# Performance work log

Hardware: AMD Instinct MI355X
Metric: run time of the kernel (lower is better)

The kernel has to match this reference:

```python
import jax, jax.numpy as jnp
import numpy as np
from jax import lax

H = 256       # GRU/LSTM hidden size
E = 32        # word embedding dim
VOCAB = 128000
MAX_EP = 1000
P_LEN, C_LEN, N_LEN = 512, 256, 512
FH = FW = 6
IMG_FLAT = 64 * FH * FW  # 2304


def _gru(xs, wih, whh, bih, bhh):
    # torch nn.GRU semantics, gate order [r; z; n]; xs: (T, E) -> (T, H)
    gi = xs @ wih.T + bih  # (T, 3H), precompute input projections
    def step(h, g):
        gh = h @ whh.T + bhh
        ir, iz, inn = jnp.split(g, 3)
        hr, hz, hn = jnp.split(gh, 3)
        r = jax.nn.sigmoid(ir + hr)
        z = jax.nn.sigmoid(iz + hz)
        n = jnp.tanh(inn + r * hn)
        h2 = (1.0 - z) * n + z * h
        return h2, h2
    _, hs = lax.scan(step, jnp.zeros((H,), xs.dtype), gi)
    return hs


def _conv(x, w, b, s):
    y = lax.conv_general_dilated(x, w, (s, s), 'VALID',
                                 dimension_numbers=('NCHW', 'OIHW', 'NCHW'))
    return y + b[None, :, None, None]


def setup_inputs() -> dict:
    key = jax.random.key(0)
    ks = iter(jax.random.split(key, 64))
    def w(shape, s=0.02):
        return jax.random.normal(next(ks), shape, jnp.float32) * s
    inp = {}
    inp['x'] = jax.random.normal(next(ks), (1, 3, 124, 124), jnp.float32)
    inp['hx'] = jax.random.normal(next(ks), (1, H), jnp.float32) * 0.1
    inp['cx'] = jax.random.normal(next(ks), (1, H), jnp.float32) * 0.1
    inp['prev_inst'] = jax.random.randint(next(ks), (1, P_LEN), 0, VOCAB)
    inp['curr_inst'] = jax.random.randint(next(ks), (1, C_LEN), 0, VOCAB)
    inp['next_inst'] = jax.random.randint(next(ks), (1, N_LEN), 0, VOCAB)
    inp['tx'] = jax.random.randint(next(ks), (1,), 0, MAX_EP + 1)
    # parameters
    inp['emb'] = w((VOCAB, E), 0.05)
    # GRU order: [f_prev, f_curr, f_next, b_prev, b_curr, b_next]
    inp['gru_wih'] = w((6, 3 * H, E))
    inp['gru_whh'] = w((6, 3 * H, H))
    inp['gru_bih'] = w((6, 3 * H), 0.01)
    inp['gru_bhh'] = w((6, 3 * H), 0.01)
    inp['conv1_w'] = w((128, 3, 8, 8));   inp['conv1_b'] = w((128,), 0.01)
    inp['conv2_w'] = w((64, 128, 4, 4));  inp['conv2_b'] = w((64,), 0.01)
    inp['conv3_w'] = w((64, 64, 4, 4));   inp['conv3_b'] = w((64,), 0.01)
    inp['img_w'] = w((256, IMG_FLAT));    inp['img_b'] = w((256,), 0.01)
    inp['akp_w'] = w((256, 768));         inp['akp_b'] = w((256,), 0.01)
    inp['akn_w'] = w((256, 768));         inp['akn_b'] = w((256,), 0.01)
    inp['bil_p_w'] = w((1, 256, 512));    inp['bil_p_b'] = w((1,), 0.01)
    inp['bil_n_w'] = w((1, 256, 512));    inp['bil_n_b'] = w((1,), 0.01)
    inp['pred_w'] = w((64, 512));         inp['pred_b'] = w((64,), 0.01)
    inp['nred_w'] = w((64, 512));         inp['nred_b'] = w((64,), 0.01)
    inp['gate_w'] = w((64, 512 + 128));   inp['gate_b'] = w((64,), 0.01)
    inp['lin_w'] = w((256, IMG_FLAT));    inp['lin_b'] = w((256,), 0.01)
    inp['lstm_wih'] = w((4 * H, 256));    inp['lstm_whh'] = w((4 * H, H))
    inp['lstm_bih'] = jnp.zeros((4 * H,), jnp.float32)
    inp['lstm_bhh'] = jnp.zeros((4 * H,), jnp.float32)
    inp['time_emb'] = w((MAX_EP + 1, E), 0.05)
    inp['crit_w'] = w((1, 256 + E));      inp['crit_b'] = jnp.zeros((1,), jnp.float32)
    inp['act_w'] = w((4, 256 + E), 0.01); inp['act_b'] = jnp.zeros((4,), jnp.float32)
    return inp


def reference(x, hx, cx, prev_inst, curr_inst, next_inst, tx, emb,
              gru_wih, gru_whh, gru_bih, gru_bhh,
              conv1_w, conv1_b, conv2_w, conv2_b, conv3_w, conv3_b,
              img_w, img_b, akp_w, akp_b, akn_w, akn_b,
              bil_p_w, bil_p_b, bil_n_w, bil_n_b,
              pred_w, pred_b, nred_w, nred_b, gate_w, gate_b,
              lin_w, lin_b, lstm_wih, lstm_whh, lstm_bih, lstm_bhh,
              time_emb, crit_w, crit_b, act_w, act_b):
    # CNN tower
    x1 = jax.nn.relu(_conv(x, conv1_w, conv1_b, 4))
    x2 = jax.nn.relu(_conv(x1, conv2_w, conv2_b, 2))
    x_img = jax.nn.relu(_conv(x2, conv3_w, conv3_b, 2))  # (1,64,6,6)

    ep = emb[prev_inst[0]]  # (P, E)
    ec = emb[curr_inst[0]]  # (C, E)
    en = emb[next_inst[0]]  # (N, E)
    P, C, N = ep.shape[0], ec.shape[0], en.shape[0]

    def run(j, e):
        return _gru(e, gru_wih[j], gru_whh[j], gru_bih[j], gru_bhh[j])
    hf = jnp.concatenate([run(0, ep), run(1, ec), run(2, en)], 0)  # (T, H)
    hb = jnp.concatenate([run(3, ep), run(4, ec), run(5, en)], 0)
    rb = hb[::-1]  # source reverses only the collected hidden list

    curr_rep = jnp.concatenate([hf[P + C - 1], rb[P]])[None]        # (1, 512)
    prev_rep = jnp.concatenate([hf[:P], rb[:P]], 1)                  # (P, 512)
    next_rep = jnp.concatenate([hf[P + C:], rb[P + C:]], 1)          # (N, 512)

    image_emb = x_img.reshape(1, -1) @ img_w.T + img_b               # (1, 256)
    ak_in = jnp.concatenate([curr_rep, image_emb], 1)                # (1, 768)

    def attend(ak_w, ak_b, bw, bb, rep):
        k = (ak_in @ ak_w.T + ak_b)[0]           # (256,) shared key
        s = (k @ bw[0]) @ rep.T + bb[0]          # (L,) bilinear scores
        wgt = jax.nn.softmax(s)
        return wgt @ rep                          # (512,)

    prev_sum = attend(akp_w, akp_b, bil_p_w, bil_p_b, prev_rep)
    next_sum = attend(akn_w, akn_b, bil_n_w, bil_n_b, next_rep)
    pg = prev_sum @ pred_w.T + pred_b            # (64,)
    ng = next_sum @ nred_w.T + nred_b            # (64,)

    gate_in = jnp.concatenate([curr_rep[0], pg, ng])[None]  # (1, 640)
    gate = jax.nn.sigmoid(gate_in @ gate_w.T + gate_b)      # (1, 64)

    xg = (x_img * gate[:, :, None, None]).reshape(1, -1)
    feat = jax.nn.relu(xg @ lin_w.T + lin_b)                # (1, 256)

    # torch LSTMCell, gate order [i; f; g; o]
    g = feat @ lstm_wih.T + lstm_bih + hx @ lstm_whh.T + lstm_bhh
    i, f, gg, o = jnp.split(g, 4, axis=1)
    cx2 = jax.nn.sigmoid(f) * cx + jax.nn.sigmoid(i) * jnp.tanh(gg)
    hx2 = jax.nn.sigmoid(o) * jnp.tanh(cx2)

    te = time_emb[tx].reshape(1, E)
    z = jnp.concatenate([hx2, te], 1)                       # (1, 288)
    return (z @ crit_w.T + crit_b, z @ act_w.T + act_b, hx2, cx2)
```

## Files before the change

### kernel.cpp

```cpp
#include <hip/hip_runtime.h>
#include <hip/hip_bf16.h>

typedef unsigned int u32;
typedef _Float16 f16x8 __attribute__((ext_vector_type(8)));
typedef float f32x4 __attribute__((ext_vector_type(4)));

__device__ __forceinline__ float sigf(float x){ return 1.0f/(1.0f + __expf(-x)); }
__device__ __forceinline__ float tanhfast(float x){
  float xc = fminf(fmaxf(x, -15.0f), 15.0f);
  float e = __expf(2.0f*xc);
  return (e - 1.0f)/(e + 1.0f);
}

#define GI_OFF   0
#define GI_SZ    (2560*768)
#define HF_OFF   (GI_OFF + GI_SZ)
#define HF_SZ    (1280*256)
#define HB_OFF   (HF_OFF + HF_SZ)
#define X1_OFF   (HB_OFF + HF_SZ)
#define X1_SZ    (128*30*30)
#define X2_OFF   (X1_OFF + X1_SZ)
#define X2_SZ    (64*14*14)
#define XIMG_OFF (X2_OFF + X2_SZ)
#define XIMG_SZ  (64*6*6)
#define AKIN_OFF (XIMG_OFF + XIMG_SZ)
#define PSUM_OFF (AKIN_OFF + 768)
#define NSUM_OFF (PSUM_OFF + 512)
#define GATE_OFF (NSUM_OFF + 512)
#define FEAT_OFF (GATE_OFF + 64)
#define G_OFF    (FEAT_OFF + 256)

__global__ __launch_bounds__(256) void gi_kernel(
    const float* __restrict__ emb, const float* __restrict__ wih_all,
    const float* __restrict__ bih_all,
    const int* __restrict__ prev, const int* __restrict__ curr, const int* __restrict__ nxt,
    float* __restrict__ gi_all)
{
  const int offs[7] = {0,512,768,1280,1792,2048,2560};
  int row0 = blockIdx.x * 16;
  int j = 0;
  while (row0 >= offs[j+1]) ++j;
  int t0 = row0 - offs[j];
  int sel = j % 3;
  const int* inst = (sel==0)? prev : (sel==1)? curr : nxt;

  __shared__ __align__(16) float e[16][32];
  int u = threadIdx.x;
  for (int idx=u; idx<512; idx+=256){
    int r = idx >> 5, k = idx & 31;
    e[r][k] = emb[(size_t)inst[t0+r]*32 + k];
  }
  __syncthreads();

  const float* wih = wih_all + (size_t)j*768*32;
  const float* bih = bih_all + (size_t)j*768;
  for (int g3=0; g3<3; ++g3){
    int o = g3*256 + u;
    float bb = bih[o];
    float acc[16];
#pragma unroll
    for (int r=0;r<16;++r) acc[r]=bb;
    const float* wr = wih + (size_t)o*32;
#pragma unroll
    for (int k=0;k<32;++k){
      float w = wr[k];
#pragma unroll
      for (int r=0;r<16;++r) acc[r] += w * e[r][k];
    }
    for (int r=0;r<16;++r) gi_all[(size_t)(row0+r)*768 + o] = acc[r];
  }
}

__global__ __launch_bounds__(256,1) void gru_scan_kernel(
    const float* __restrict__ whh_all, const float* __restrict__ bhh_all,
    const float* __restrict__ gi_all, float* __restrict__ hf, float* __restrict__ hb)
{
  const int lens[6] = {512,256,512,512,256,512};
  const int offs[6] = {0,512,768,1280,1792,2048};
  int j = blockIdx.x;
  int u = threadIdx.x;
  int len = lens[j];
  const float* gi = gi_all + (size_t)offs[j]*768;
  float* outp = ((j<3)? hf : hb) + (size_t)offs[j%3]*256;

  int w    = u >> 6;
  int l    = u & 63;
  int arow = l & 15;
  int kgrp = l >> 4;

  f16x8 af[12][8];
  {
    const float* Wj = whh_all + (size_t)j*768*256;
#pragma unroll
    for (int i=0;i<12;++i){
      const float* wrow = Wj + (size_t)(16*(w*12+i) + arow)*256;
#pragma unroll
      for (int kt=0;kt<8;++kt){
        const float4* p = (const float4*)(wrow + 32*kt + 8*kgrp);
        float4 c0 = p[0], c1 = p[1];
        f16x8 v;
        v[0]=(_Float16)c0.x; v[1]=(_Float16)c0.y; v[2]=(_Float16)c0.z; v[3]=(_Float16)c0.w;
        v[4]=(_Float16)c1.x; v[5]=(_Float16)c1.y; v[6]=(_Float16)c1.z; v[7]=(_Float16)c1.w;
        af[i][kt] = v;
      }
    }
  }

  float bh0 = bhh_all[j*768 + u];
  float bh1 = bhh_all[j*768 + 256 + u];
  float bh2 = bhh_all[j*768 + 512 + u];
  float hprev = 0.0f;

  __shared__ __align__(16) _Float16 h16[256];
  __shared__ __align__(16) float gacc[768];
  h16[u] = (_Float16)0.0f;
  __syncthreads();

  for (int t=0; t<len; ++t){
    if (t > 0) outp[(size_t)(t-1)*256 + u] = hprev;
    const float* git = gi + (size_t)t*768;
    float gr = git[u], gz = git[256+u], gn = git[512+u];

#pragma unroll
    for (int g=0; g<3; ++g){
      f32x4 acc[4];
#pragma unroll
      for (int i=0;i<4;++i){ f32x4 zz = {0.f,0.f,0.f,0.f}; acc[i] = zz; }
#pragma unroll
      for (int kt=0; kt<8; ++kt){
        f16x8 bfr = *(const f16x8*)(h16 + 32*kt + 8*kgrp);
#pragma unroll
        for (int i=0;i<4;++i)
          acc[i] = __builtin_amdgcn_mfma_f32_16x16x32_f16(af[g*4+i][kt], bfr, acc[i], 0, 0, 0);
      }
      if (arow == 0){
#pragma unroll
        for (int i=0;i<4;++i){
          float4 v; v.x=acc[i][0]; v.y=acc[i][1]; v.z=acc[i][2]; v.w=acc[i][3];
          *(float4*)&gacc[16*(w*12 + g*4 + i) + 4*kgrp] = v;
        }
      }
    }
    __syncthreads();

    float r  = sigf(gr + bh0 + gacc[u]);
    float z  = sigf(gz + bh1 + gacc[256+u]);
    float n  = tanhfast(gn + bh2 + r*gacc[512+u]);
    float h2 = (1.0f - z)*n + z*hprev;
    h16[u] = (_Float16)h2;
    hprev = h2;
    __syncthreads();
  }
  outp[(size_t)(len-1)*256 + u] = hprev;
}

__global__ __launch_bounds__(256) void conv1_kernel(
    const float* __restrict__ x, const float* __restrict__ w, const float* __restrict__ b,
    float* __restrict__ y)
{
  int idx = blockIdx.x*256 + threadIdx.x;
  if (idx >= 128*30*30) return;
  int c = idx/900, rem = idx%900, i = rem/30, jx = rem%30;
  float acc = b[c];
  const float* wc = w + (size_t)c*3*8*8;
  for (int ic=0; ic<3; ++ic)
    for (int ky=0; ky<8; ++ky){
      const float* xrow = x + ((size_t)ic*124 + (i*4+ky))*124 + jx*4;
      const float* wrow = wc + (ic*8+ky)*8;
#pragma unroll
      for (int kx=0; kx<8; ++kx) acc += xrow[kx] * wrow[kx];
    }
  y[idx] = fmaxf(acc, 0.0f);
}

__global__ __launch_bounds__(256) void conv2_kernel(
    const float* __restrict__ x1, const float* __restrict__ w, const float* __restrict__ b,
    float* __restrict__ y)
{
  int idx = blockIdx.x*256 + threadIdx.x;
  if (idx >= 64*14*14) return;
  int c = idx/196, rem = idx%196, i = rem/14, jx = rem%14;
  float acc = b[c];
  for (int ic=0; ic<128; ++ic){
    const float* xc = x1 + (size_t)ic*900;
    const float* wc = w + ((size_t)c*128 + ic)*16;
#pragma unroll
    for (int ky=0; ky<4; ++ky)
#pragma unroll
      for (int kx=0; kx<4; ++kx)
        acc += xc[(i*2+ky)*30 + (jx*2+kx)] * wc[ky*4+kx];
  }
  y[idx] = fmaxf(acc, 0.0f);
}

__global__ __launch_bounds__(256) void conv3_kernel(
    const float* __restrict__ x2, const float* __restrict__ w, const float* __restrict__ b,
    float* __restrict__ y)
{
  int idx = blockIdx.x*256 + threadIdx.x;
  if (idx >= 64*6*6) return;
  int c = idx/36, rem = idx%36, i = rem/6, jx = rem%6;
  float acc = b[c];
  for (int ic=0; ic<64; ++ic){
    const float* xc = x2 + (size_t)ic*196;
    const float* wc = w + ((size_t)c*64 + ic)*16;
#pragma unroll
    for (int ky=0; ky<4; ++ky)
#pragma unroll
      for (int kx=0; kx<4; ++kx)
        acc += xc[(i*2+ky)*14 + (jx*2+kx)] * wc[ky*4+kx];
  }
  y[idx] = fmaxf(acc, 0.0f);
}

__global__ __launch_bounds__(256) void imgemb_kernel(
    const float* __restrict__ x_img, const float* __restrict__ img_w, const float* __restrict__ img_b,
    const float* __restrict__ hf, const float* __restrict__ hb, float* __restrict__ ak_in)
{
  int u = threadIdx.x;
  int r = blockIdx.x*8 + (u>>5);
  int lane = u & 31;
  const float* wr = img_w + (size_t)r*2304;
  float acc = 0.0f;
  for (int k=lane; k<2304; k+=32) acc += wr[k]*x_img[k];
#pragma unroll
  for (int m=16; m; m>>=1) acc += __shfl_xor(acc, m, 64);
  if (lane == 0) ak_in[512+r] = img_b[r] + acc;
  if (blockIdx.x == 0){
    ak_in[u]     = hf[(size_t)767*256+u];
    ak_in[256+u] = hb[(size_t)767*256+u];
  }
}

__global__ __launch_bounds__(512) void attend_kernel(
    const float* __restrict__ ak_in_g,
    const float* __restrict__ akp_w, const float* __restrict__ akp_b,
    const float* __restrict__ akn_w, const float* __restrict__ akn_b,
    const float* __restrict__ bil_p_w, const float* __restrict__ bil_p_b,
    const float* __restrict__ bil_n_w, const float* __restrict__ bil_n_b,
    const float* __restrict__ hf, const float* __restrict__ hb,
    float* __restrict__ prev_sum, float* __restrict__ next_sum)
{
  int blk = blockIdx.x;
  const float* akw = blk? akn_w : akp_w;
  const float* akb = blk? akn_b : akp_b;
  const float* bw  = blk? bil_n_w : bil_p_w;
  float bb         = blk? bil_n_b[0] : bil_p_b[0];
  float* outp      = blk? next_sum : prev_sum;

  int u = threadIdx.x;
  __shared__ __align__(16) float ak[768];
  __shared__ __align__(16) float kk[256];
  __shared__ __align__(16) float q[512];
  __shared__ float s[512], red[512];

  for (int i=u; i<768; i+=512) ak[i] = ak_in_g[i];
  __syncthreads();

  if (u < 256){
    float a0=0.f,a1=0.f,a2=0.f,a3=0.f;
    const float4* wr = (const float4*)(akw + (size_t)u*768);
    const float4* av = (const float4*)ak;
    for (int m=0; m<192; ++m){
      float4 w = wr[m], aa = av[m];
      a0 += w.x*aa.x; a1 += w.y*aa.y; a2 += w.z*aa.z; a3 += w.w*aa.w;
    }
    kk[u] = akb[u] + ((a0+a1)+(a2+a3));
  }
  __syncthreads();

  {
    float acc = 0.0f;
    for (int m=0; m<256; ++m) acc += kk[m]*bw[(size_t)m*512 + u];
    q[u] = acc;
  }
  __syncthreads();

  {
    int i = u;
    const float4* repf = (const float4*)(hf + (size_t)(blk? (768+i) : i)*256);
    const float4* repb = (const float4*)(hb + (size_t)(blk? (511-i) : (1279-i))*256);
    const float4* qf = (const float4*)q;
    float a0=0.f,a1=0.f;
    for (int v=0; v<64; ++v){
      float4 qq = qf[v],  rr = repf[v];
      a0 += qq.x*rr.x + qq.y*rr.y + qq.z*rr.z + qq.w*rr.w;
      float4 q2 = qf[64+v], r2 = repb[v];
      a1 += q2.x*r2.x + q2.y*r2.y + q2.z*r2.z + q2.w*r2.w;
    }
    s[u] = bb + a0 + a1;
  }
  __syncthreads();

  red[u] = s[u]; __syncthreads();
  for (int st=256; st>0; st>>=1){ if (u<st) red[u]=fmaxf(red[u],red[u+st]); __syncthreads(); }
  float mx = red[0]; __syncthreads();
  float ex = __expf(s[u]-mx);
  red[u] = ex; __syncthreads();
  for (int st=256; st>0; st>>=1){ if (u<st) red[u]+=red[u+st]; __syncthreads(); }
  float inv = 1.0f/red[0]; __syncthreads();
  s[u] = ex*inv;
  __syncthreads();

  float o = 0.0f;
  if (u < 256){
    for (int r=0; r<512; ++r){
      const float* rf = hf + (size_t)(blk? (768+r) : r)*256;
      o += s[r]*rf[u];
    }
    outp[u] = o;
  } else {
    int v = u-256;
    for (int r=0; r<512; ++r){
      const float* rb = hb + (size_t)(blk? (511-r) : (1279-r))*256;
      o += s[r]*rb[v];
    }
    outp[u] = o;
  }
}

__global__ __launch_bounds__(256) void head_a_kernel(
    const float* __restrict__ psum, const float* __restrict__ nsum,
    const float* __restrict__ akin,
    const float* __restrict__ pred_w, const float* __restrict__ pred_b,
    const float* __restrict__ nred_w, const float* __restrict__ nred_b,
    const float* __restrict__ gate_w, const float* __restrict__ gate_b,
    float* __restrict__ gate_out)
{
  int u = threadIdx.x;
  __shared__ __align__(16) float ps[512], ns[512], cr[512];
  __shared__ float pg[64], ng[64];
  for (int i=u; i<512; i+=256){ ps[i]=psum[i]; ns[i]=nsum[i]; cr[i]=akin[i]; }
  __syncthreads();

  if (u < 64){
    float a = pred_b[u];
    const float* wr = pred_w + (size_t)u*512;
    for (int k=0;k<512;++k) a += ps[k]*wr[k];
    pg[u] = a;
  } else if (u < 128){
    int t = u-64;
    float a = nred_b[t];
    const float* wr = nred_w + (size_t)t*512;
    for (int k=0;k<512;++k) a += ns[k]*wr[k];
    ng[t] = a;
  }
  __syncthreads();

  if (u < 64){
    float a = gate_b[u];
    const float* wr = gate_w + (size_t)u*640;
    for (int k=0;k<512;++k) a += cr[k]*wr[k];
    for (int k=0;k<64;++k)  a += pg[k]*wr[512+k];
    for (int k=0;k<64;++k)  a += ng[k]*wr[576+k];
    gate_out[u] = sigf(a);
  }
}

__global__ __launch_bounds__(256) void lin_kernel(
    const float* __restrict__ x_img, const float* __restrict__ gate,
    const float* __restrict__ lin_w, const float* __restrict__ lin_b,
    float* __restrict__ feat)
{
  int u = threadIdx.x;
  __shared__ __align__(16) float xg[2304];
  for (int i=u; i<2304; i+=256) xg[i] = x_img[i]*gate[i/36];
  __syncthreads();

  int r = blockIdx.x*8 + (u>>5);
  int lane = u & 31;
  const float* wr = lin_w + (size_t)r*2304;
  float acc = 0.0f;
  for (int k=lane; k<2304; k+=32) acc += wr[k]*xg[k];
#pragma unroll
  for (int m=16; m; m>>=1) acc += __shfl_xor(acc, m, 64);
  if (lane == 0) feat[r] = fmaxf(lin_b[r] + acc, 0.0f);
}

__global__ __launch_bounds__(256) void lstm_kernel(
    const float* __restrict__ feat, const float* __restrict__ hx,
    const float* __restrict__ wih, const float* __restrict__ whh,
    const float* __restrict__ bih, const float* __restrict__ bhh,
    float* __restrict__ g)
{
  int u = threadIdx.x;
  __shared__ __align__(16) float fs[256], hs[256];
  fs[u] = feat[u]; hs[u] = hx[u];
  __syncthreads();
  int row = blockIdx.x*256 + u;
  float a0=0.f, a1=0.f;
  const float4* w1 = (const float4*)(wih + (size_t)row*256);
  const float4* w2 = (const float4*)(whh + (size_t)row*256);
  const float4* fv = (const float4*)fs;
  const float4* hv = (const float4*)hs;
  for (int k=0;k<64;++k){
    float4 wa = w1[k], fa = fv[k];
    a0 += wa.x*fa.x + wa.y*fa.y + wa.z*fa.z + wa.w*fa.w;
    float4 wb = w2[k], ha = hv[k];
    a1 += wb.x*ha.x + wb.y*ha.y + wb.z*ha.z + wb.w*ha.w;
  }
  g[row] = bih[row] + bhh[row] + a0 + a1;
}

__global__ __launch_bounds__(320) void final_kernel(
    const float* __restrict__ g, const float* __restrict__ cx,
    const int* __restrict__ tx, const float* __restrict__ time_emb,
    const float* __restrict__ crit_w, const float* __restrict__ crit_b,
    const float* __restrict__ act_w,  const float* __restrict__ act_b,
    float* __restrict__ out)
{
  int u = threadIdx.x;
  __shared__ float z[320];
  if (u < 256){
    float ii=g[u], ff=g[256+u], gg=g[512+u], oo=g[768+u];
    float c2 = sigf(ff)*cx[u] + sigf(ii)*tanhfast(gg);
    float h2 = sigf(oo)*tanhfast(c2);
    out[5+u]   = h2;
    out[261+u] = c2;
    z[u] = h2;
  } else if (u < 288){
    z[u] = time_emb[(size_t)tx[0]*32 + (u-256)];
  }
  __syncthreads();
  int row = u >> 6, lane = u & 63;
  const float* wv = (row==0)? crit_w : (act_w + (size_t)(row-1)*288);
  float acc = 0.0f;
  for (int k=lane; k<288; k+=64) acc += wv[k]*z[k];
#pragma unroll
  for (int m=32; m; m>>=1) acc += __shfl_xor(acc, m, 64);
  if (lane == 0){
    float b = (row==0)? crit_b[0] : act_b[row-1];
    out[row] = acc + b;
  }
}

extern "C" void kernel_launch(void* const* d_in, const int* in_sizes, int n_in,
                              void* d_out, int out_size, void* d_ws, size_t ws_size,
                              hipStream_t stream)
{
  const float* x        = (const float*)d_in[0];
  const float* hx       = (const float*)d_in[1];
  const float* cx       = (const float*)d_in[2];
  const int*  prev      = (const int*)d_in[3];
  const int*  curr      = (const int*)d_in[4];
  const int*  nxt       = (const int*)d_in[5];
  const int*  tx        = (const int*)d_in[6];
  const float* emb      = (const float*)d_in[7];
  const float* gru_wih  = (const float*)d_in[8];
  const float* gru_whh  = (const float*)d_in[9];
  const float* gru_bih  = (const float*)d_in[10];
  const float* gru_bhh  = (const float*)d_in[11];
  const float* conv1_w  = (const float*)d_in[12];
  const float* conv1_b  = (const float*)d_in[13];
  const float* conv2_w  = (const float*)d_in[14];
  const float* conv2_b  = (const float*)d_in[15];
  const float* conv3_w  = (const float*)d_in[16];
  const float* conv3_b  = (const float*)d_in[17];
  const float* img_w    = (const float*)d_in[18];
  const float* img_b    = (const float*)d_in[19];
  const float* akp_w    = (const float*)d_in[20];
  const float* akp_b    = (const float*)d_in[21];
  const float* akn_w    = (const float*)d_in[22];
  const float* akn_b    = (const float*)d_in[23];
  const float* bil_p_w  = (const float*)d_in[24];
  const float* bil_p_b  = (const float*)d_in[25];
  const float* bil_n_w  = (const float*)d_in[26];
  const float* bil_n_b  = (const float*)d_in[27];
  const float* pred_w   = (const float*)d_in[28];
  const float* pred_b   = (const float*)d_in[29];
  const float* nred_w   = (const float*)d_in[30];
  const float* nred_b   = (const float*)d_in[31];
  const float* gate_w   = (const float*)d_in[32];
  const float* gate_b   = (const float*)d_in[33];
  const float* lin_w    = (const float*)d_in[34];
  const float* lin_b    = (const float*)d_in[35];
  const float* lstm_wih = (const float*)d_in[36];
  const float* lstm_whh = (const float*)d_in[37];
  const float* lstm_bih = (const float*)d_in[38];
  const float* lstm_bhh = (const float*)d_in[39];
  const float* time_emb = (const float*)d_in[40];
  const float* crit_w   = (const float*)d_in[41];
  const float* crit_b   = (const float*)d_in[42];
  const float* act_w    = (const float*)d_in[43];
  const float* act_b    = (const float*)d_in[44];

  float* ws = (float*)d_ws;
  float* gi    = ws + GI_OFF;
  float* hf    = ws + HF_OFF;
  float* hb    = ws + HB_OFF;
  float* x1    = ws + X1_OFF;
  float* x2    = ws + X2_OFF;
  float* ximg  = ws + XIMG_OFF;
  float* akin  = ws + AKIN_OFF;
  float* psum  = ws + PSUM_OFF;
  float* nsum  = ws + NSUM_OFF;
  float* gatev = ws + GATE_OFF;
  float* featv = ws + FEAT_OFF;
  float* gvec  = ws + G_OFF;

  float* out = (float*)d_out;

  gi_kernel      <<<160, 256, 0, stream>>>(emb, gru_wih, gru_bih, prev, curr, nxt, gi);
  gru_scan_kernel<<<6,   256, 0, stream>>>(gru_whh, gru_bhh, gi, hf, hb);
  conv1_kernel   <<<450, 256, 0, stream>>>(x, conv1_w, conv1_b, x1);
  conv2_kernel   <<<49,  256, 0, stream>>>(x1, conv2_w, conv2_b, x2);
  conv3_kernel   <<<9,   256, 0, stream>>>(x2, conv3_w, conv3_b, ximg);
  imgemb_kernel  <<<32,  256, 0, stream>>>(ximg, img_w, img_b, hf, hb, akin);
  attend_kernel  <<<2,   512, 0, stream>>>(akin, akp_w, akp_b, akn_w, akn_b,
                                           bil_p_w, bil_p_b, bil_n_w, bil_n_b,
                                           hf, hb, psum, nsum);
  head_a_kernel  <<<1,   256, 0, stream>>>(psum, nsum, akin,
                                           pred_w, pred_b, nred_w, nred_b,
                                           gate_w, gate_b, gatev);
  lin_kernel     <<<32,  256, 0, stream>>>(ximg, gatev, lin_w, lin_b, featv);
  lstm_kernel    <<<4,   256, 0, stream>>>(featv, hx, lstm_wih, lstm_whh,
                                           lstm_bih, lstm_bhh, gvec);
  final_kernel   <<<1,   320, 0, stream>>>(gvec, cx, tx, time_emb,
                                           crit_w, crit_b, act_w, act_b, out);
}
```

Baseline: 1.098 ms.

## Split GRU recurrent matvec across 8 waves instead of 4

The GRU scan block grows from 256 to 512 threads, so each of the 8 waves holds 6 MFMA row tiles of the recurrent weight matrix instead of 12. This halves each wave's serial MFMA chain per timestep and per-thread register pressure. The elementwise gate update runs only on the first 256 threads, which leaves the extra waves idle during that phase. The cost is more threads taking part in the two barriers per step.

```diff
diff --git a/kernel.cpp b/kernel.cpp
--- a/kernel.cpp
+++ b/kernel.cpp
@@ -71,7 +71,10 @@
   }
 }
 
-__global__ __launch_bounds__(256,1) void gru_scan_kernel(
+__global__
+__attribute__((amdgpu_flat_work_group_size(512,512)))
+__attribute__((amdgpu_waves_per_eu(2,2)))
+void gru_scan_kernel(
     const float* __restrict__ whh_all, const float* __restrict__ bhh_all,
     const float* __restrict__ gi_all, float* __restrict__ hf, float* __restrict__ hb)
 {
@@ -88,12 +91,12 @@
   int arow = l & 15;
   int kgrp = l >> 4;
 
-  f16x8 af[12][8];
+  f16x8 af[6][8];
   {
     const float* Wj = whh_all + (size_t)j*768*256;
 #pragma unroll
-    for (int i=0;i<12;++i){
-      const float* wrow = Wj + (size_t)(16*(w*12+i) + arow)*256;
+    for (int i=0;i<6;++i){
+      const float* wrow = Wj + (size_t)(16*(w*6+i) + arow)*256;
 #pragma unroll
       for (int kt=0;kt<8;++kt){
         const float4* p = (const float4*)(wrow + 32*kt + 8*kgrp);
@@ -106,52 +109,56 @@
     }
   }
 
-  float bh0 = bhh_all[j*768 + u];
-  float bh1 = bhh_all[j*768 + 256 + u];
-  float bh2 = bhh_all[j*768 + 512 + u];
-  float hprev = 0.0f;
+  float bh0=0.f, bh1=0.f, bh2=0.f, hprev=0.f;
+  if (u < 256){
+    bh0 = bhh_all[j*768 + u];
+    bh1 = bhh_all[j*768 + 256 + u];
+    bh2 = bhh_all[j*768 + 512 + u];
+  }
 
   __shared__ __align__(16) _Float16 h16[256];
   __shared__ __align__(16) float gacc[768];
-  h16[u] = (_Float16)0.0f;
+  if (u < 256) h16[u] = (_Float16)0.0f;
   __syncthreads();
 
   for (int t=0; t<len; ++t){
-    if (t > 0) outp[(size_t)(t-1)*256 + u] = hprev;
-    const float* git = gi + (size_t)t*768;
-    float gr = git[u], gz = git[256+u], gn = git[512+u];
-
-#pragma unroll
-    for (int g=0; g<3; ++g){
-      f32x4 acc[4];
-#pragma unroll
-      for (int i=0;i<4;++i){ f32x4 zz = {0.f,0.f,0.f,0.f}; acc[i] = zz; }
-#pragma unroll
-      for (int kt=0; kt<8; ++kt){
-        f16x8 bfr = *(const f16x8*)(h16 + 32*kt + 8*kgrp);
-#pragma unroll
-        for (int i=0;i<4;++i)
-          acc[i] = __builtin_amdgcn_mfma_f32_16x16x32_f16(af[g*4+i][kt], bfr, acc[i], 0, 0, 0);
+    float gr=0.f, gz=0.f, gn=0.f;
+    if (u < 256){
+      if (t > 0) outp[(size_t)(t-1)*256 + u] = hprev;
+      const float* git = gi + (size_t)t*768;
+      gr = git[u]; gz = git[256+u]; gn = git[512+u];
+    }
+
+    f32x4 acc[6];
+#pragma unroll
+    for (int i=0;i<6;++i){ f32x4 zz = {0.f,0.f,0.f,0.f}; acc[i] = zz; }
+#pragma unroll
+    for (int kt=0; kt<8; ++kt){
+      f16x8 bfr = *(const f16x8*)(h16 + 32*kt + 8*kgrp);
+#pragma unroll
+      for (int i=0;i<6;++i)
+        acc[i] = __builtin_amdgcn_mfma_f32_16x16x32_f16(af[i][kt], bfr, acc[i], 0, 0, 0);
+    }
+    if (arow == 0){
+#pragma unroll
+      for (int i=0;i<6;++i){
+        float4 v; v.x=acc[i][0]; v.y=acc[i][1]; v.z=acc[i][2]; v.w=acc[i][3];
+        *(float4*)&gacc[16*(w*6+i) + 4*kgrp] = v;
       }
-      if (arow == 0){
-#pragma unroll
-        for (int i=0;i<4;++i){
-          float4 v; v.x=acc[i][0]; v.y=acc[i][1]; v.z=acc[i][2]; v.w=acc[i][3];
-          *(float4*)&gacc[16*(w*12 + g*4 + i) + 4*kgrp] = v;
-        }
-      }
     }
     __syncthreads();
 
-    float r  = sigf(gr + bh0 + gacc[u]);
-    float z  = sigf(gz + bh1 + gacc[256+u]);
-    float n  = tanhfast(gn + bh2 + r*gacc[512+u]);
-    float h2 = (1.0f - z)*n + z*hprev;
-    h16[u] = (_Float16)h2;
-    hprev = h2;
+    if (u < 256){
+      float r  = sigf(gr + bh0 + gacc[u]);
+      float z  = sigf(gz + bh1 + gacc[256+u]);
+      float n  = tanhfast(gn + bh2 + r*gacc[512+u]);
+      float h2 = (1.0f - z)*n + z*hprev;
+      h16[u] = (_Float16)h2;
+      hprev = h2;
+    }
     __syncthreads();
   }
-  outp[(size_t)(len-1)*256 + u] = hprev;
+  if (u < 256) outp[(size_t)(len-1)*256 + u] = hprev;
 }
 
 __global__ __launch_bounds__(256) void conv1_kernel(
@@ -501,7 +508,7 @@
   float* out = (float*)d_out;
 
   gi_kernel      <<<160, 256, 0, stream>>>(emb, gru_wih, gru_bih, prev, curr, nxt, gi);
-  gru_scan_kernel<<<6,   256, 0, stream>>>(gru_whh, gru_bhh, gi, hf, hb);
+  gru_scan_kernel<<<6,   512, 0, stream>>>(gru_whh, gru_bhh, gi, hf, hb);
   conv1_kernel   <<<450, 256, 0, stream>>>(x, conv1_w, conv1_b, x1);
   conv2_kernel   <<<49,  256, 0, stream>>>(x1, conv2_w, conv2_b, x2);
   conv3_kernel   <<<9,   256, 0, stream>>>(x2, conv3_w, conv3_b, ximg);
```

Result: faster. 950.9 us (-13.4%).
